# Performance work log

Hardware: AMD Instinct MI355X
Metric: run time of the kernel (lower is better)

Reference implementation:

```python
import jax, jax.numpy as jnp
import numpy as np

GROUP_SIZE = 128


def _unpack_int4(packed):
    # packed: [..., P] int32, each holding 8 int4 nibbles (LSB-first).
    u = jax.lax.bitcast_convert_type(packed, jnp.uint32)
    shifts = jnp.arange(8, dtype=jnp.uint32) * 4  # nibble bit offsets
    vals = (u[..., None] >> shifts) & jnp.uint32(15)  # [..., P, 8]
    return vals.reshape(*packed.shape[:-1], -1)  # [..., P*8] in [0, 15]


def setup_inputs() -> dict:
    key = jax.random.key(0)
    k1, k2, k3, k4 = jax.random.split(key, 4)
    B, S, K, O = 4, 16, 4096, 11008
    G = K // GROUP_SIZE          # 32 groups
    GP = (G + 7) // 8            # 4 packed-zero columns
    imax = np.iinfo(np.int32).max
    x = jax.random.normal(k1, (B, S, K), dtype=jnp.float16)
    qweight_i32 = jax.random.randint(k2, (O, K // 8), 0, imax, dtype=jnp.int32)
    qzeros_i32 = jax.random.randint(k3, (O, GP), 0, imax, dtype=jnp.int32)
    scales_f16 = jax.random.uniform(k4, (O, G), dtype=jnp.float16,
                                    minval=0.001, maxval=0.02)
    return {"x": x, "qweight_i32": qweight_i32, "qzeros_i32": qzeros_i32,
            "scales_f16": scales_f16}


def reference(x, qweight_i32, qzeros_i32, scales_f16):
    O, G = scales_f16.shape
    K = G * GROUP_SIZE
    # Dequantize: w = (q - z) * s, per-group int4 quantization.
    q = _unpack_int4(qweight_i32)[:, :K].astype(jnp.float16)       # [O, K]
    z = _unpack_int4(qzeros_i32)[:, :G].astype(jnp.float16)        # [O, G]
    z_k = jnp.repeat(z, GROUP_SIZE, axis=1)                        # [O, K]
    s_k = jnp.repeat(scales_f16, GROUP_SIZE, axis=1)               # [O, K]
    w = (q - z_k) * s_k                                            # fp16 [O, K]
    x2d = x.reshape(-1, K).astype(jnp.float16)                     # [m, K]
    out = jnp.matmul(x2d, w.T).astype(jnp.float32)                 # [m, O]
    return out.reshape(*x.shape[:-1], O)
```

## Files before the change

### kernel.cpp

```cpp
#include <hip/hip_runtime.h>
#include <stdint.h>

typedef _Float16 half8  __attribute__((ext_vector_type(8)));
typedef float    floatx4 __attribute__((ext_vector_type(4)));
typedef uint32_t uint4v  __attribute__((ext_vector_type(4)));

#define KDIM 4096
#define ODIM 11008
#define NG   32
#define KSPLIT 4
#define GPB  8
#define OBLK 172
#define PART_ELEMS (64 * ODIM)

__device__ __forceinline__ uint32_t pk_f16(float a, float b) {
    return __builtin_bit_cast(uint32_t, __builtin_amdgcn_cvt_pkrtz(a, b));
}

__device__ __forceinline__ void async16(uint32_t* lds, const uint32_t* g) {
    __builtin_amdgcn_global_load_lds(
        (const __attribute__((address_space(1))) uint32_t*)(uintptr_t)g,
        (__attribute__((address_space(3))) uint32_t*)(uintptr_t)lds,
        16, 0, 0);
}

__global__ __launch_bounds__(256) void cvt_x_kernel(
    const float4* __restrict__ x, uint4v* __restrict__ xh2,
    float* __restrict__ xsumT)
{
    const int i = blockIdx.x * 256 + threadIdx.x;
    const float4 f0 = x[2 * i];
    const float4 f1 = x[2 * i + 1];
    const uint4v v = {pk_f16(f0.x, f1.x), pk_f16(f0.y, f1.y),
                      pk_f16(f0.z, f1.z), pk_f16(f0.w, f1.w)};
    const int m  = i >> 9, c = i & 511;
    const int g  = c >> 4, cg = c & 15, q = cg >> 2, ks = cg & 3;
    const int mt = m >> 4, ml = m & 15;
    xh2[((size_t)(g * 4 + ks) * 4 + mt) * 64 + q * 16 + ml] = v;

    float p = f0.x + f0.y + f0.z + f0.w + f1.x + f1.y + f1.z + f1.w;
    p += __shfl_xor(p, 1);
    p += __shfl_xor(p, 2);
    p += __shfl_xor(p, 4);
    p += __shfl_xor(p, 8);
    if ((threadIdx.x & 15) == 0) xsumT[g * 64 + m] = p;
}

__global__ __launch_bounds__(256) void reduce_kernel(
    const float4* __restrict__ part, float4* __restrict__ out)
{
    const int NT = OBLK * 256;
    for (int i = blockIdx.x * 256 + threadIdx.x; i < PART_ELEMS / 4; i += NT) {
        float4 a = part[i];
        #pragma unroll
        for (int kb = 1; kb < KSPLIT; ++kb) {
            const float4 b = part[(size_t)kb * (PART_ELEMS / 4) + i];
            a.x += b.x; a.y += b.y; a.z += b.z; a.w += b.w;
        }
        out[i] = a;
    }
}

__global__ __launch_bounds__(256, 4) void w4a16_kernel(
    const uint4v*   __restrict__ xh2,
    const uint32_t* __restrict__ qw,
    const uint32_t* __restrict__ qz,
    const float*    __restrict__ sc,
    const float*    __restrict__ xsumT,
    float*          __restrict__ part)
{
    __shared__ uint32_t qlds[GPB * 4 * 256];

    const int t    = threadIdx.x;
    const int wv   = t >> 6;
    const int lane = t & 63;
    const int q    = lane >> 4;
    const int ml   = lane & 15;

    const int kb = blockIdx.x & 3;
    const int ob = blockIdx.x >> 2;
    const int o0 = ob * 64;

    #pragma unroll
    for (int i = 0; i < 8; ++i) {
        const int idx = wv * 8 + i;
        const int g   = idx >> 2;
        const int sub = idx & 3;
        const uint32_t* ga = qw + (size_t)(o0 + sub * 16 + ml) * 512
                                + kb * 128 + g * 16 + q * 4;
        async16(&qlds[idx * 256], ga);
    }

    const uint4v* xp = xh2 + ((size_t)(kb * 32) * 4 + wv) * 64 + lane;
    uint4v ax[2][4];
    #pragma unroll
    for (int ks = 0; ks < 4; ++ks) ax[0][ks] = xp[ks * 256];

    uint32_t zdw[4];
    #pragma unroll
    for (int sub = 0; sub < 4; ++sub)
        zdw[sub] = qz[(size_t)(o0 + sub * 16 + ml) * 4 + kb];
    const float* scp = sc + (size_t)(o0 + ml) * NG + kb * 8;

    const int mrow = wv * 16 + q * 4;
    floatx4 acc[4] = {{0.f,0.f,0.f,0.f},{0.f,0.f,0.f,0.f},
                      {0.f,0.f,0.f,0.f},{0.f,0.f,0.f,0.f}};

    __syncthreads();

    #pragma unroll
    for (int g = 0; g < GPB; ++g) {
        if (g + 1 < GPB) {
            #pragma unroll
            for (int ks = 0; ks < 4; ++ks)
                ax[(g + 1) & 1][ks] = xp[(size_t)((g + 1) * 16 + ks * 4) * 64];
        }

        const floatx4 xsg = *reinterpret_cast<const floatx4*>(
            xsumT + (size_t)(kb * 8 + g) * 64 + mrow);

        #pragma unroll
        for (int sub = 0; sub < 4; ++sub) {
            const uint4v qf = *reinterpret_cast<const uint4v*>(
                &qlds[(g * 4 + sub) * 256 + lane * 4]);
            const float    s   = scp[sub * 512 + g];
            const uint32_t zn  = (zdw[sub] >> (g * 4)) & 0xFu;
            const float    czs = s * (1024.0f + (float)zn);

            floatx4 tmp = {0.f, 0.f, 0.f, 0.f};
            #pragma unroll
            for (int ks = 0; ks < 4; ++ks) {
                const uint32_t ud = qf[ks];
                const uint4v bw = {
                    ( ud         & 0x000F000Fu) | 0x64006400u,
                    ((ud >> 4)   & 0x000F000Fu) | 0x64006400u,
                    ((ud >> 8)   & 0x000F000Fu) | 0x64006400u,
                    ((ud >> 12)  & 0x000F000Fu) | 0x64006400u};
                const half8 b = __builtin_bit_cast(half8, bw);
                tmp = __builtin_amdgcn_mfma_f32_16x16x32_f16(
                    __builtin_bit_cast(half8, ax[g & 1][ks]), b, tmp, 0, 0, 0);
            }
            #pragma unroll
            for (int r = 0; r < 4; ++r)
                acc[sub][r] += s * tmp[r] - czs * xsg[r];
        }
    }

    float* pb = part + (size_t)kb * PART_ELEMS + (size_t)mrow * ODIM;
    #pragma unroll
    for (int sub = 0; sub < 4; ++sub) {
        float* op = pb + o0 + sub * 16 + ml;
        op[0]                = acc[sub][0];
        op[(size_t)ODIM]     = acc[sub][1];
        op[2 * (size_t)ODIM] = acc[sub][2];
        op[3 * (size_t)ODIM] = acc[sub][3];
    }
}

extern "C" void kernel_launch(void* const* d_in, const int* in_sizes, int n_in,
                              void* d_out, int out_size, void* d_ws, size_t ws_size,
                              hipStream_t stream) {
    const float*    x       = (const float*)d_in[0];
    const uint32_t* qweight = (const uint32_t*)d_in[1];
    const uint32_t* qzeros  = (const uint32_t*)d_in[2];
    const float*    scales  = (const float*)d_in[3];
    float* out = (float*)d_out;

    uint4v* xh2   = (uint4v*)d_ws;
    float*  xsumT = (float*)((char*)d_ws + 512 * 1024);
    float*  part  = (float*)((char*)d_ws + 1024 * 1024);

    cvt_x_kernel<<<dim3(128), dim3(256), 0, stream>>>((const float4*)x, xh2, xsumT);
    w4a16_kernel<<<dim3(OBLK * KSPLIT), dim3(256), 0, stream>>>(
        xh2, qweight, qzeros, scales, xsumT, part);
    reduce_kernel<<<dim3(OBLK), dim3(256), 0, stream>>>(
        (const float4*)part, (float4*)out);
}
```

Measured before the change: 113.3 us.

## Drop split-K and reduce kernel; stream full-K weights through double-buffered LDS

Removes the 4-way K split and its separate reduction kernel. Each block now covers 32 output columns across all of K and writes final results directly. Weights are staged through a padded, double-buffered LDS tile using register prefetch, with a sync per pair of groups. This saves the partial-sum write/read traffic and one kernel launch. In exchange there are only 344 blocks, fewer than the 688 before, each running a longer serial loop with 16 barriers, which may reduce parallelism on a 256-CU device.

```diff
diff --git a/kernel.cpp b/kernel.cpp
--- a/kernel.cpp
+++ b/kernel.cpp
@@ -8,20 +8,12 @@
 #define KDIM 4096
 #define ODIM 11008
 #define NG   32
-#define KSPLIT 4
-#define GPB  8
-#define OBLK 172
-#define PART_ELEMS (64 * ODIM)
+#define OT   32
+#define NBLK (ODIM / OT)
+#define LPITCH 36
 
 __device__ __forceinline__ uint32_t pk_f16(float a, float b) {
     return __builtin_bit_cast(uint32_t, __builtin_amdgcn_cvt_pkrtz(a, b));
-}
-
-__device__ __forceinline__ void async16(uint32_t* lds, const uint32_t* g) {
-    __builtin_amdgcn_global_load_lds(
-        (const __attribute__((address_space(1))) uint32_t*)(uintptr_t)g,
-        (__attribute__((address_space(3))) uint32_t*)(uintptr_t)lds,
-        16, 0, 0);
 }
 
 __global__ __launch_bounds__(256) void cvt_x_kernel(
@@ -46,110 +38,94 @@
     if ((threadIdx.x & 15) == 0) xsumT[g * 64 + m] = p;
 }
 
-__global__ __launch_bounds__(256) void reduce_kernel(
-    const float4* __restrict__ part, float4* __restrict__ out)
-{
-    const int NT = OBLK * 256;
-    for (int i = blockIdx.x * 256 + threadIdx.x; i < PART_ELEMS / 4; i += NT) {
-        float4 a = part[i];
-        #pragma unroll
-        for (int kb = 1; kb < KSPLIT; ++kb) {
-            const float4 b = part[(size_t)kb * (PART_ELEMS / 4) + i];
-            a.x += b.x; a.y += b.y; a.z += b.z; a.w += b.w;
-        }
-        out[i] = a;
-    }
-}
-
-__global__ __launch_bounds__(256, 4) void w4a16_kernel(
+__global__ __launch_bounds__(256, 2) void w4a16_kernel(
     const uint4v*   __restrict__ xh2,
     const uint32_t* __restrict__ qw,
     const uint32_t* __restrict__ qz,
     const float*    __restrict__ sc,
     const float*    __restrict__ xsumT,
-    float*          __restrict__ part)
+    float*          __restrict__ out)
 {
-    __shared__ uint32_t qlds[GPB * 4 * 256];
+    __shared__ uint32_t qlds[2][OT * LPITCH];
 
     const int t    = threadIdx.x;
     const int wv   = t >> 6;
     const int lane = t & 63;
     const int q    = lane >> 4;
     const int ml   = lane & 15;
+    const int o0   = blockIdx.x * OT;
 
-    const int kb = blockIdx.x & 3;
-    const int ob = blockIdx.x >> 2;
-    const int o0 = ob * 64;
+    const int r = t >> 3, c = t & 7;
+    const uint32_t* sgp = qw + (size_t)(o0 + r) * 512 + c * 4;
+    const int widx = r * LPITCH + c * 4;
 
-    #pragma unroll
-    for (int i = 0; i < 8; ++i) {
-        const int idx = wv * 8 + i;
-        const int g   = idx >> 2;
-        const int sub = idx & 3;
-        const uint32_t* ga = qw + (size_t)(o0 + sub * 16 + ml) * 512
-                                + kb * 128 + g * 16 + q * 4;
-        async16(&qlds[idx * 256], ga);
-    }
+    uint4v ureg[2];
+    ureg[0] = *reinterpret_cast<const uint4v*>(sgp);
+    ureg[1] = *reinterpret_cast<const uint4v*>(sgp + 32);
 
-    const uint4v* xp = xh2 + ((size_t)(kb * 32) * 4 + wv) * 64 + lane;
+    const uint4v* xp = xh2 + (size_t)wv * 64 + lane;
     uint4v ax[2][4];
     #pragma unroll
     for (int ks = 0; ks < 4; ++ks) ax[0][ks] = xp[ks * 256];
 
-    uint32_t zdw[4];
+    uint4v zr[2];
     #pragma unroll
-    for (int sub = 0; sub < 4; ++sub)
-        zdw[sub] = qz[(size_t)(o0 + sub * 16 + ml) * 4 + kb];
-    const float* scp = sc + (size_t)(o0 + ml) * NG + kb * 8;
+    for (int sub = 0; sub < 2; ++sub)
+        zr[sub] = *reinterpret_cast<const uint4v*>(
+            qz + (size_t)(o0 + sub * 16 + ml) * 4);
 
     const int mrow = wv * 16 + q * 4;
-    floatx4 acc[4] = {{0.f,0.f,0.f,0.f},{0.f,0.f,0.f,0.f},
-                      {0.f,0.f,0.f,0.f},{0.f,0.f,0.f,0.f}};
-
-    __syncthreads();
+    floatx4 acc[2] = {{0.f,0.f,0.f,0.f},{0.f,0.f,0.f,0.f}};
 
     #pragma unroll
-    for (int g = 0; g < GPB; ++g) {
-        if (g + 1 < GPB) {
-            #pragma unroll
-            for (int ks = 0; ks < 4; ++ks)
-                ax[(g + 1) & 1][ks] = xp[(size_t)((g + 1) * 16 + ks * 4) * 64];
-        }
-
-        const floatx4 xsg = *reinterpret_cast<const floatx4*>(
-            xsumT + (size_t)(kb * 8 + g) * 64 + mrow);
+    for (int gp = 0; gp < 16; ++gp) {
+        *reinterpret_cast<uint4v*>(&qlds[gp & 1][widx]) = ureg[gp & 1];
+        __syncthreads();
+        if (gp + 2 < 16)
+            ureg[gp & 1] = *reinterpret_cast<const uint4v*>(sgp + (gp + 2) * 32);
 
         #pragma unroll
-        for (int sub = 0; sub < 4; ++sub) {
-            const uint4v qf = *reinterpret_cast<const uint4v*>(
-                &qlds[(g * 4 + sub) * 256 + lane * 4]);
-            const float    s   = scp[sub * 512 + g];
-            const uint32_t zn  = (zdw[sub] >> (g * 4)) & 0xFu;
-            const float    czs = s * (1024.0f + (float)zn);
+        for (int gi = 0; gi < 2; ++gi) {
+            const int g = gp * 2 + gi;
+            if (g + 1 < 32) {
+                #pragma unroll
+                for (int ks = 0; ks < 4; ++ks)
+                    ax[(g + 1) & 1][ks] = xp[(size_t)((g + 1) * 4 + ks) * 256];
+            }
+            const floatx4 xsg = *reinterpret_cast<const floatx4*>(
+                xsumT + g * 64 + mrow);
 
-            floatx4 tmp = {0.f, 0.f, 0.f, 0.f};
             #pragma unroll
-            for (int ks = 0; ks < 4; ++ks) {
-                const uint32_t ud = qf[ks];
-                const uint4v bw = {
-                    ( ud         & 0x000F000Fu) | 0x64006400u,
-                    ((ud >> 4)   & 0x000F000Fu) | 0x64006400u,
-                    ((ud >> 8)   & 0x000F000Fu) | 0x64006400u,
-                    ((ud >> 12)  & 0x000F000Fu) | 0x64006400u};
-                const half8 b = __builtin_bit_cast(half8, bw);
-                tmp = __builtin_amdgcn_mfma_f32_16x16x32_f16(
-                    __builtin_bit_cast(half8, ax[g & 1][ks]), b, tmp, 0, 0, 0);
+            for (int sub = 0; sub < 2; ++sub) {
+                const uint4v qf = *reinterpret_cast<const uint4v*>(
+                    &qlds[gp & 1][(sub * 16 + ml) * LPITCH + gi * 16 + q * 4]);
+                const float    s  = sc[(size_t)(o0 + sub * 16 + ml) * NG + g];
+                const uint32_t zn = (zr[sub][g >> 3] >> ((g & 7) * 4)) & 0xFu;
+                const float    czs = s * (1024.0f + (float)zn);
+
+                floatx4 tmp = {0.f, 0.f, 0.f, 0.f};
+                #pragma unroll
+                for (int ks = 0; ks < 4; ++ks) {
+                    const uint32_t ud = qf[ks];
+                    const uint4v bw = {
+                        ( ud         & 0x000F000Fu) | 0x64006400u,
+                        ((ud >> 4)   & 0x000F000Fu) | 0x64006400u,
+                        ((ud >> 8)   & 0x000F000Fu) | 0x64006400u,
+                        ((ud >> 12)  & 0x000F000Fu) | 0x64006400u};
+                    const half8 b = __builtin_bit_cast(half8, bw);
+                    tmp = __builtin_amdgcn_mfma_f32_16x16x32_f16(
+                        __builtin_bit_cast(half8, ax[g & 1][ks]), b, tmp, 0, 0, 0);
+                }
+                #pragma unroll
+                for (int rr = 0; rr < 4; ++rr)
+                    acc[sub][rr] += s * tmp[rr] - czs * xsg[rr];
             }
-            #pragma unroll
-            for (int r = 0; r < 4; ++r)
-                acc[sub][r] += s * tmp[r] - czs * xsg[r];
         }
     }
 
-    float* pb = part + (size_t)kb * PART_ELEMS + (size_t)mrow * ODIM;
     #pragma unroll
-    for (int sub = 0; sub < 4; ++sub) {
-        float* op = pb + o0 + sub * 16 + ml;
+    for (int sub = 0; sub < 2; ++sub) {
+        float* op = out + (size_t)mrow * ODIM + o0 + sub * 16 + ml;
         op[0]                = acc[sub][0];
         op[(size_t)ODIM]     = acc[sub][1];
         op[2 * (size_t)ODIM] = acc[sub][2];
@@ -168,11 +144,8 @@
 
     uint4v* xh2   = (uint4v*)d_ws;
     float*  xsumT = (float*)((char*)d_ws + 512 * 1024);
-    float*  part  = (float*)((char*)d_ws + 1024 * 1024);
 
     cvt_x_kernel<<<dim3(128), dim3(256), 0, stream>>>((const float4*)x, xh2, xsumT);
-    w4a16_kernel<<<dim3(OBLK * KSPLIT), dim3(256), 0, stream>>>(
-        xh2, qweight, qzeros, scales, xsumT, part);
-    reduce_kernel<<<dim3(OBLK), dim3(256), 0, stream>>>(
-        (const float4*)part, (float4*)out);
+    w4a16_kernel<<<dim3(NBLK), dim3(256), 0, stream>>>(
+        xh2, qweight, qzeros, scales, xsumT, out);
 }
```

Result: slower. 164.3 us (+45.0%).
